# Performance work log

Hardware: AMD Instinct MI355X
Metric: run time of the kernel (lower is better)

Reference implementation:

```python
import jax, jax.numpy as jnp
import numpy as np

NEG = 1e9  # mask value added to already-selected positions (original uses -1e9)


def setup_inputs() -> dict:
    key = jax.random.key(0)
    ks = jax.random.split(key, 12)
    B, N, M = 8, 2048, 256
    s = 0.05  # keep gates/softmax in a sane range
    return dict(
        node_embedding=jax.random.normal(ks[0], (B, N, M), dtype=jnp.float32),
        z_g=jax.random.normal(ks[1], (B, M), dtype=jnp.float32) * s,
        decoder_init=jax.random.normal(ks[2], (M,), dtype=jnp.float32) * s,
        hidden0=jax.random.normal(ks[3], (M,), dtype=jnp.float32) * s,
        w_ih=jax.random.normal(ks[4], (4 * M, M), dtype=jnp.float32) * s,
        w_hh=jax.random.normal(ks[5], (4 * M, M), dtype=jnp.float32) * s,
        b_ih=jax.random.normal(ks[6], (4 * M,), dtype=jnp.float32) * s,
        b_hh=jax.random.normal(ks[7], (4 * M,), dtype=jnp.float32) * s,
        Wq=jax.random.normal(ks[8], (M, M), dtype=jnp.float32) * s,
        bq=jax.random.normal(ks[9], (M,), dtype=jnp.float32) * s,
        Wk=jax.random.normal(ks[10], (M, M), dtype=jnp.float32) * s,
        bk=jax.random.normal(ks[11], (M,), dtype=jnp.float32) * s,
    )


def reference(node_embedding, z_g, decoder_init, hidden0,
              w_ih, w_hh, b_ih, b_hh, Wq, bq, Wk, bk):
    # Returns the per-step masked softmax attention distributions [B, N, N]
    # (row t = distribution over boxes at decode step t; argmax of each row
    #  is the predicted order, and selected indices are masked out).
    N = node_embedding.shape[1]
    # LSTM input is the constant decoder_init every step -> precompute its proj.
    x_proj = decoder_init @ w_ih.T + b_ih  # [4M]

    def decode_one(z_g_b, node_emb_b):
        keys = node_emb_b @ Wk.T + bk  # [N, M] (self.key(node_embedding))

        def step(carry, _):
            h, c, used = carry
            # torch LSTMCell: gates ordered (i, f, g, o)
            gates = x_proj + h @ w_hh.T + b_hh  # [4M]
            i_g, f_g, g_g, o_g = jnp.split(gates, 4)
            i_g = jax.nn.sigmoid(i_g)
            f_g = jax.nn.sigmoid(f_g)
            g_g = jnp.tanh(g_g)
            o_g = jax.nn.sigmoid(o_g)
            c = f_g * c + i_g * g_g
            h = o_g * jnp.tanh(c)
            q = h @ Wq.T + bq                    # [M]
            scores = keys @ q                    # [N]
            scores = jnp.where(used, scores - NEG, scores)  # mask selected
            probs = jax.nn.softmax(scores)       # [N]
            idx = jnp.argmax(probs)              # top-1 pointer selection
            used = used.at[idx].set(True)
            return (h, c, used), probs

        init = (hidden0, z_g_b, jnp.zeros((N,), dtype=bool))
        _, probs = jax.lax.scan(step, init, None, length=N)
        return probs  # [N, N]

    return jax.vmap(decode_one)(z_g, node_embedding)  # [B, N, N]
```

## Files before the change

### kernel.cpp

```cpp
#include <hip/hip_runtime.h>
#include <cstdint>
#include <cstddef>

#define NB 8
#define NN 2048
#define MM 256

typedef unsigned long long u64;

__device__ __forceinline__ unsigned mapf(float f) {
  unsigned u = __float_as_uint(f + 0.f);
  return ((int)u >= 0) ? (u ^ 0x80000000u) : ~u;
}
__device__ __forceinline__ u64 shflx_u64(u64 v, int m) {
  unsigned lo = (unsigned)__shfl_xor((int)(unsigned)v, m);
  unsigned hi = (unsigned)__shfl_xor((int)(v >> 32), m);
  return ((u64)hi << 32) | lo;
}

__global__ __launch_bounds__(1024) void lstm_kernel(
    const float* __restrict__ z_g, const float* __restrict__ dec,
    const float* __restrict__ h0, const float* __restrict__ w_ih,
    const float* __restrict__ w_hh, const float* __restrict__ b_ih,
    const float* __restrict__ b_hh, const float* __restrict__ Wq,
    const float* __restrict__ bq, float* __restrict__ Qout,
    u64* __restrict__ Hslow)
{
  const int b = blockIdx.x;
  const int j = blockIdx.y;
  const int tid = threadIdx.x;
  const int w = tid >> 6;
  const int lane = tid & 63;
  const int q = w & 7;
  const int rg = w >> 3;
  const int lr = rg * 64 + lane;
  const int g = lr >> 5;
  const int mi = lr & 31;
  const int grow = g * 256 + 32 * j + mi;

  __shared__ __align__(16) float part[2][8][128];
  __shared__ __align__(16) float part2[2][32][33];

  float wreg[32];
  {
    const float* wr = w_hh + (size_t)grow * MM + 32 * q;
    #pragma unroll
    for (int i = 0; i < 8; ++i) {
      float4 v = *(const float4*)(wr + 4 * i);
      wreg[4 * i + 0] = v.x; wreg[4 * i + 1] = v.y;
      wreg[4 * i + 2] = v.z; wreg[4 * i + 3] = v.w;
    }
  }
  float wqa[8];
  {
    const float* wr = Wq + (size_t)(32 * j + mi) * MM + 32 * q + 8 * g;
    float4 w0 = *(const float4*)(wr);
    float4 w1 = *(const float4*)(wr + 4);
    wqa[0] = w0.x; wqa[1] = w0.y; wqa[2] = w0.z; wqa[3] = w0.w;
    wqa[4] = w1.x; wqa[5] = w1.y; wqa[6] = w1.z; wqa[7] = w1.w;
  }
  const float bqv = (w == 1 && lane < 32) ? bq[32 * j + lane] : 0.f;

  {
    float p = 0.f;
    const float* wr = w_ih + (size_t)grow * MM + 32 * q;
    #pragma unroll
    for (int i = 0; i < 8; ++i) {
      float4 wv = *(const float4*)(wr + 4 * i);
      float4 dv = *(const float4*)(dec + 32 * q + 4 * i);
      p += wv.x * dv.x + wv.y * dv.y + wv.z * dv.z + wv.w * dv.w;
    }
    part[0][q][lr] = p;
  }
  __syncthreads();

  float xbA = 0.f, xbB = 0.f, c_my = 0.f;
  if (w == 0) {
    #pragma unroll
    for (int rr = 0; rr < 2; ++rr) {
      const int lr2 = lane + rr * 64;
      const int g2 = lr2 >> 5, mi2 = lr2 & 31;
      const int grow2 = g2 * 256 + 32 * j + mi2;
      float xb = b_ih[grow2] + b_hh[grow2];
      #pragma unroll
      for (int qq = 0; qq < 8; ++qq) xb += part[0][qq][lr2];
      if (rr == 0) xbA = xb; else xbB = xb;
    }
    if (lane < 32) c_my = z_g[b * MM + 32 * j + lane];
  }
  __syncthreads();

  u64* Hs = Hslow + (size_t)b * 512;
  const int hidx = 32 * q + (lane & 31);

  for (int t = 0; t <= NN; ++t) {
    int hvi;
    if (t == 0) {
      hvi = __float_as_int(h0[hidx]);
    } else {
      const int off = ((t & 1) << 8) + hidx;
      u64 v = __hip_atomic_load(Hs + off, __ATOMIC_RELAXED,
                                __HIP_MEMORY_SCOPE_AGENT);
      for (;;) {
        if (__all((int)((unsigned)(v >> 32) == (unsigned)t))) break;
        v = __hip_atomic_load(Hs + off, __ATOMIC_RELAXED,
                              __HIP_MEMORY_SCOPE_AGENT);
      }
      hvi = (int)(unsigned)v;
    }

    {
      float a0 = 0.f, a1 = 0.f, a2 = 0.f, a3 = 0.f;
      #pragma unroll
      for (int k = 0; k < 32; k += 4) {
        a0 = fmaf(__uint_as_float((unsigned)__builtin_amdgcn_readlane(hvi, k + 0)), wreg[k + 0], a0);
        a1 = fmaf(__uint_as_float((unsigned)__builtin_amdgcn_readlane(hvi, k + 1)), wreg[k + 1], a1);
        a2 = fmaf(__uint_as_float((unsigned)__builtin_amdgcn_readlane(hvi, k + 2)), wreg[k + 2], a2);
        a3 = fmaf(__uint_as_float((unsigned)__builtin_amdgcn_readlane(hvi, k + 3)), wreg[k + 3], a3);
      }
      part[t & 1][q][lr] = (a0 + a1) + (a2 + a3);
    }

    {
      float qa = 0.f;
      #pragma unroll
      for (int i = 0; i < 8; ++i) {
        const float hh = __uint_as_float((unsigned)__shfl(hvi, 8 * g + i));
        qa = fmaf(hh, wqa[i], qa);
      }
      if (t > 0) part2[t & 1][g * 8 + q][mi] = qa;
    }
    __syncthreads();

    if (w == 0 && t < NN) {
      float vA = xbA, vB = xbB;
      #pragma unroll
      for (int qq = 0; qq < 8; ++qq) {
        vA += part[t & 1][qq][lane];
        vB += part[t & 1][qq][lane + 64];
      }
      const float s1 = 1.f / (1.f + __expf(-vA));
      const float e  = __expf(((lane < 32) ? -2.f : -1.f) * vB);
      const float s2 = (lane < 32) ? (2.f / (1.f + e) - 1.f)
                                   : (1.f / (1.f + e));
      const float fo1 = __shfl_xor(s1, 32);
      const float fo2 = __shfl_xor(s2, 32);
      if (lane < 32) {
        c_my = fo1 * c_my + s1 * s2;
        const float e2 = __expf(-2.f * c_my);
        const float hn = fo2 * (2.f / (1.f + e2) - 1.f);
        const u64 pk = ((u64)(unsigned)(t + 1) << 32) | (u64)__float_as_uint(hn);
        const int so = (((t + 1) & 1) << 8) + 32 * j + lane;
        __hip_atomic_store(Hs + so, pk, __ATOMIC_RELAXED,
                           __HIP_MEMORY_SCOPE_AGENT);
      }
    }

    if (w == 1 && t > 0 && lane < 32) {
      float s = 0.f;
      #pragma unroll
      for (int p = 0; p < 32; ++p) s += part2[t & 1][p][lane];
      Qout[((size_t)b * NN + (t - 1)) * MM + 32 * j + lane] = s + bqv;
    }
  }
}

__global__ __launch_bounds__(256) void gemm128(
    const float* __restrict__ A, const float* __restrict__ B,
    float* __restrict__ C, const float* __restrict__ bias,
    int K, int Ncol, long sA, long sB, long sC)
{
  __shared__ __align__(16) float As[32][132];
  __shared__ __align__(16) float Bs[32][132];
  const int tid = threadIdx.x;
  const int tx = tid & 15;
  const int ty = tid >> 4;
  const int row0 = blockIdx.y * 128;
  const int col0 = blockIdx.x * 128;
  const float* Ab = A + (size_t)blockIdx.z * (size_t)sA;
  const float* Bb = B + (size_t)blockIdx.z * (size_t)sB;
  float* Cb = C + (size_t)blockIdx.z * (size_t)sC;

  float acc[8][8];
  #pragma unroll
  for (int i = 0; i < 8; ++i)
    #pragma unroll
    for (int jj = 0; jj < 8; ++jj) acc[i][jj] = 0.f;

  for (int k0 = 0; k0 < K; k0 += 32) {
    #pragma unroll
    for (int it = 0; it < 4; ++it) {
      const int idx = tid + it * 256;
      const int r = idx >> 3;
      const int c4 = (idx & 7) << 2;
      float4 va = *(const float4*)(Ab + (size_t)(row0 + r) * K + k0 + c4);
      float4 vb = *(const float4*)(Bb + (size_t)(col0 + r) * K + k0 + c4);
      As[c4 + 0][r] = va.x; As[c4 + 1][r] = va.y;
      As[c4 + 2][r] = va.z; As[c4 + 3][r] = va.w;
      Bs[c4 + 0][r] = vb.x; Bs[c4 + 1][r] = vb.y;
      Bs[c4 + 2][r] = vb.z; Bs[c4 + 3][r] = vb.w;
    }
    __syncthreads();
    #pragma unroll
    for (int kk = 0; kk < 32; ++kk) {
      float4 a0 = *(const float4*)&As[kk][ty * 4];
      float4 a1 = *(const float4*)&As[kk][64 + ty * 4];
      float4 b0 = *(const float4*)&Bs[kk][tx * 4];
      float4 b1 = *(const float4*)&Bs[kk][64 + tx * 4];
      const float av[8] = {a0.x, a0.y, a0.z, a0.w, a1.x, a1.y, a1.z, a1.w};
      const float bv[8] = {b0.x, b0.y, b0.z, b0.w, b1.x, b1.y, b1.z, b1.w};
      #pragma unroll
      for (int i = 0; i < 8; ++i)
        #pragma unroll
        for (int jj = 0; jj < 8; ++jj)
          acc[i][jj] = fmaf(av[i], bv[jj], acc[i][jj]);
    }
    __syncthreads();
  }

  #pragma unroll
  for (int i = 0; i < 8; ++i) {
    const int r = row0 + ((i < 4) ? (ty * 4 + i) : (64 + ty * 4 + i - 4));
    float* cp = Cb + (size_t)r * Ncol + col0;
    float4 o0, o1;
    float* o0p = &o0.x; float* o1p = &o1.x;
    #pragma unroll
    for (int jj = 0; jj < 4; ++jj) {
      float v0 = acc[i][jj], v1 = acc[i][jj + 4];
      if (bias) {
        v0 += bias[col0 + tx * 4 + jj];
        v1 += bias[col0 + 64 + tx * 4 + jj];
      }
      o0p[jj] = v0; o1p[jj] = v1;
    }
    *(float4*)(cp + tx * 4) = o0;
    *(float4*)(cp + 64 + tx * 4) = o1;
  }
}

__global__ __launch_bounds__(512) void select_block(
    const float* __restrict__ S, int* __restrict__ sel)
{
  const int b = blockIdx.x;
  const int tid = threadIdx.x;
  const int w = tid >> 6;
  const int lane = tid & 63;
  const float* Sb = S + (size_t)b * NN * NN + 4 * tid;
  int* selb = sel + b * NN;

  __shared__ u64 partial[2][8];

  for (int i = tid; i < NN; i += 512) selb[i] = 0x7fffffff;
  __syncthreads();

  unsigned mybits = 0;
  const unsigned base = 2047u - 4u * (unsigned)tid;

  auto stepf = [&](float4 v, int t) {
    u64 k0 = (mybits & 1u) ? 0 : (((u64)mapf(v.x) << 32) | (base - 0u));
    u64 k1 = (mybits & 2u) ? 0 : (((u64)mapf(v.y) << 32) | (base - 1u));
    u64 k2 = (mybits & 4u) ? 0 : (((u64)mapf(v.z) << 32) | (base - 2u));
    u64 k3 = (mybits & 8u) ? 0 : (((u64)mapf(v.w) << 32) | (base - 3u));
    u64 k = k0 > k1 ? k0 : k1;
    if (k2 > k) k = k2;
    if (k3 > k) k = k3;
    #pragma unroll
    for (int off = 1; off < 64; off <<= 1) {
      u64 o = shflx_u64(k, off);
      if (o > k) k = o;
    }
    if (lane == 0) partial[t & 1][w] = k;
    __syncthreads();
    u64 pk = partial[t & 1][lane & 7];
    #pragma unroll
    for (int off = 1; off < 8; off <<= 1) {
      u64 o = shflx_u64(pk, off);
      if (o > pk) pk = o;
    }
    const int idx = 2047 - (int)(pk & 0x7ff);
    if ((idx >> 2) == tid) mybits |= 1u << (idx & 3);
    if (tid == 0) selb[idx] = t;
  };

  float4 r0 = *(const float4*)(Sb + (size_t)0 * NN);
  float4 r1 = *(const float4*)(Sb + (size_t)1 * NN);
  float4 r2 = *(const float4*)(Sb + (size_t)2 * NN);
  float4 r3 = *(const float4*)(Sb + (size_t)3 * NN);
  for (int t = 0; t < NN; t += 4) {
    const size_t p4 = (size_t)((t + 4 < NN) ? t + 4 : NN - 1) * NN;
    const size_t p5 = (size_t)((t + 5 < NN) ? t + 5 : NN - 1) * NN;
    const size_t p6 = (size_t)((t + 6 < NN) ? t + 6 : NN - 1) * NN;
    const size_t p7 = (size_t)((t + 7 < NN) ? t + 7 : NN - 1) * NN;
    stepf(r0, t);     r0 = *(const float4*)(Sb + p4);
    stepf(r1, t + 1); r1 = *(const float4*)(Sb + p5);
    stepf(r2, t + 2); r2 = *(const float4*)(Sb + p6);
    stepf(r3, t + 3); r3 = *(const float4*)(Sb + p7);
  }
}

__global__ __launch_bounds__(256) void softmax_kernel(
    float* __restrict__ out, const int* __restrict__ sel)
{
  const int t = blockIdx.x;
  const int b = blockIdx.y;
  const int tid = threadIdx.x;
  float* row = out + ((size_t)b * NN + t) * NN;
  const int* selb = sel + b * NN;
  __shared__ float red[8];

  float v[8];
  int sl[8];
  #pragma unroll
  for (int u = 0; u < 2; ++u) {
    float4 f = *(const float4*)(row + u * 1024 + tid * 4);
    int4 s4 = *(const int4*)(selb + u * 1024 + tid * 4);
    v[u * 4 + 0] = f.x; v[u * 4 + 1] = f.y; v[u * 4 + 2] = f.z; v[u * 4 + 3] = f.w;
    sl[u * 4 + 0] = s4.x; sl[u * 4 + 1] = s4.y; sl[u * 4 + 2] = s4.z; sl[u * 4 + 3] = s4.w;
  }

  float mx = -3.0e38f;
  #pragma unroll
  for (int e = 0; e < 8; ++e)
    if (sl[e] >= t) mx = fmaxf(mx, v[e]);
  #pragma unroll
  for (int off = 1; off < 64; off <<= 1) mx = fmaxf(mx, __shfl_xor(mx, off));
  if ((tid & 63) == 0) red[tid >> 6] = mx;
  __syncthreads();
  mx = fmaxf(fmaxf(red[0], red[1]), fmaxf(red[2], red[3]));

  float e8[8];
  float sum = 0.f;
  #pragma unroll
  for (int e = 0; e < 8; ++e) {
    float ex = (sl[e] >= t) ? __expf(v[e] - mx) : 0.f;
    e8[e] = ex;
    sum += ex;
  }
  #pragma unroll
  for (int off = 1; off < 64; off <<= 1) sum += __shfl_xor(sum, off);
  if ((tid & 63) == 0) red[4 + (tid >> 6)] = sum;
  __syncthreads();
  sum = red[4] + red[5] + red[6] + red[7];
  const float inv = 1.f / sum;

  #pragma unroll
  for (int u = 0; u < 2; ++u) {
    float4 o;
    o.x = e8[u * 4 + 0] * inv; o.y = e8[u * 4 + 1] * inv;
    o.z = e8[u * 4 + 2] * inv; o.w = e8[u * 4 + 3] * inv;
    *(float4*)(row + u * 1024 + tid * 4) = o;
  }
}

extern "C" void kernel_launch(void* const* d_in, const int* in_sizes, int n_in,
                              void* d_out, int out_size, void* d_ws, size_t ws_size,
                              hipStream_t stream)
{
  (void)in_sizes; (void)n_in; (void)out_size; (void)ws_size;
  const float* emb  = (const float*)d_in[0];
  const float* z_g  = (const float*)d_in[1];
  const float* dec  = (const float*)d_in[2];
  const float* h0   = (const float*)d_in[3];
  const float* w_ih = (const float*)d_in[4];
  const float* w_hh = (const float*)d_in[5];
  const float* b_ih = (const float*)d_in[6];
  const float* b_hh = (const float*)d_in[7];
  const float* Wq   = (const float*)d_in[8];
  const float* bq   = (const float*)d_in[9];
  const float* Wk   = (const float*)d_in[10];
  const float* bk   = (const float*)d_in[11];
  float* out = (float*)d_out;
  float* ws  = (float*)d_ws;

  float* keys  = ws;
  float* Q     = ws + 4194304;
  u64*   Hslow = (u64*)(ws + 8396800);
  int*   sel   = (int*)(ws + 8404992);

  lstm_kernel<<<dim3(NB, 8), 1024, 0, stream>>>(
      z_g, dec, h0, w_ih, w_hh, b_ih, b_hh, Wq, bq, Q, Hslow);

  gemm128<<<dim3(MM / 128, (NB * NN) / 128, 1), 256, 0, stream>>>(
      emb, Wk, keys, bk, MM, MM, 0, 0, 0);

  gemm128<<<dim3(NN / 128, NN / 128, NB), 256, 0, stream>>>(
      Q, keys, out, nullptr, MM, NN,
      (long)NN * MM, (long)NN * MM, (long)NN * NN);

  select_block<<<NB, 512, 0, stream>>>(out, sel);

  softmax_kernel<<<dim3(NN, NB), 256, 0, stream>>>(out, sel);
}
```

Measured before the change: 5.035 ms.

## Map LSTM blocks to XCCs so each batch syncs through the local L2

Each block reads its hardware XCC id, publishes it, and blocks are reassigned so the 8 blocks of each batch sample sit on the same XCC when possible. Those groups exchange the hidden state through a second buffer, using plain stores and sc0 loads that stay in the XCC-local L2, instead of agent-scope atomics that go through the device-coherent path. The per-step cross-block handoff latency of the 2048-step recurrence is the target. Slow-path fallbacks remain, and the new code relies on undocumented cache-coherence behaviour and on every block being resident at once for the spin barrier.

```diff
diff --git a/kernel.cpp b/kernel.cpp
--- a/kernel.cpp
+++ b/kernel.cpp
@@ -16,6 +16,16 @@
   unsigned lo = (unsigned)__shfl_xor((int)(unsigned)v, m);
   unsigned hi = (unsigned)__shfl_xor((int)(v >> 32), m);
   return ((u64)hi << 32) | lo;
+}
+
+__device__ __forceinline__ u64 load_sc0(const u64* p) {
+  u64 v;
+  asm volatile("global_load_dwordx2 %0, %1, off sc0\n\ts_waitcnt vmcnt(0)"
+               : "=v"(v) : "v"(p) : "memory");
+  return v;
+}
+__device__ __forceinline__ void store_plain(u64* p, u64 v) {
+  asm volatile("global_store_dwordx2 %0, %1, off" :: "v"(p), "v"(v) : "memory");
 }
 
 __global__ __launch_bounds__(1024) void lstm_kernel(
@@ -24,13 +34,76 @@
     const float* __restrict__ w_hh, const float* __restrict__ b_ih,
     const float* __restrict__ b_hh, const float* __restrict__ Wq,
     const float* __restrict__ bq, float* __restrict__ Qout,
-    u64* __restrict__ Hslow)
+    u64* __restrict__ Hfast, u64* __restrict__ Hslow,
+    unsigned* __restrict__ xccmap)
 {
-  const int b = blockIdx.x;
-  const int j = blockIdx.y;
+  const int flat = blockIdx.x;
   const int tid = threadIdx.x;
   const int w = tid >> 6;
   const int lane = tid & 63;
+
+  unsigned myxcc;
+  asm volatile("s_getreg_b32 %0, hwreg(HW_REG_XCC_ID)" : "=s"(myxcc));
+  myxcc &= 7u;
+  if (tid == 0)
+    __hip_atomic_store(&xccmap[flat], myxcc, __ATOMIC_RELAXED,
+                       __HIP_MEMORY_SCOPE_AGENT);
+  unsigned mv;
+  for (;;) {
+    mv = __hip_atomic_load(&xccmap[lane], __ATOMIC_RELAXED,
+                           __HIP_MEMORY_SCOPE_AGENT);
+    if (__all((int)(mv != 0xFFFFFFFFu))) break;
+  }
+  mv &= 7u;
+
+  u64 bal[8];
+  #pragma unroll
+  for (int x = 0; x < 8; ++x) bal[x] = __ballot((int)(mv == (unsigned)x));
+
+  const u64 below_me = ((u64)1 << flat) - 1;
+  int acc8 = 0, my_r = 0, my_nb = 0, my_base = 0;
+  #pragma unroll
+  for (int x = 0; x < 8; ++x) {
+    int nb = __popcll(bal[x]) >> 3;
+    const int room = 8 - acc8;
+    if (nb > room) nb = room;
+    if ((unsigned)x == myxcc) {
+      my_r = __popcll(bal[x] & below_me);
+      my_nb = nb; my_base = acc8;
+    }
+    acc8 += nb;
+  }
+
+  int b, j, fastmode;
+  if (my_r < 8 * my_nb) {
+    b = my_base + (my_r >> 3);
+    j = my_r & 7;
+    fastmode = 1;
+  } else if (acc8 < 8) {
+    const u64 below_l = ((u64)1 << lane) - 1;
+    u64 balm = bal[0];
+    #pragma unroll
+    for (int x = 1; x < 8; ++x) balm = (mv == (unsigned)x) ? bal[x] : balm;
+    const int rl = __popcll(balm & below_l);
+    int acc2 = 0, nb_l = 0;
+    #pragma unroll
+    for (int x = 0; x < 8; ++x) {
+      int nb = __popcll(bal[x]) >> 3;
+      const int room = 8 - acc2;
+      if (nb > room) nb = room;
+      if ((unsigned)x == mv) nb_l = nb;
+      acc2 += nb;
+    }
+    const u64 sm = __ballot((int)(rl >= 8 * nb_l));
+    const int sr = __popcll(sm & below_me);
+    b = acc8 + (sr >> 3);
+    j = sr & 7;
+    fastmode = 0;
+    if (b >= 8) return;
+  } else {
+    return;
+  }
+
   const int q = w & 7;
   const int rg = w >> 3;
   const int lr = rg * 64 + lane;
@@ -90,6 +163,7 @@
   }
   __syncthreads();
 
+  u64* Hf = Hfast + (size_t)b * 512;
   u64* Hs = Hslow + (size_t)b * 512;
   const int hidx = 32 * q + (lane & 31);
 
@@ -97,12 +171,23 @@
     int hvi;
     if (t == 0) {
       hvi = __float_as_int(h0[hidx]);
+    } else if (fastmode) {
+      const int off = ((t & 1) << 8) + hidx;
+      u64 v = load_sc0(Hf + off);
+      int tries = 0;
+      while (!__all((int)((unsigned)(v >> 32) == (unsigned)t))) {
+        ++tries;
+        v = ((tries & 15) == 15)
+                ? __hip_atomic_load(Hs + off, __ATOMIC_RELAXED,
+                                    __HIP_MEMORY_SCOPE_AGENT)
+                : load_sc0(Hf + off);
+      }
+      hvi = (int)(unsigned)v;
     } else {
       const int off = ((t & 1) << 8) + hidx;
       u64 v = __hip_atomic_load(Hs + off, __ATOMIC_RELAXED,
                                 __HIP_MEMORY_SCOPE_AGENT);
-      for (;;) {
-        if (__all((int)((unsigned)(v >> 32) == (unsigned)t))) break;
+      while (!__all((int)((unsigned)(v >> 32) == (unsigned)t))) {
         v = __hip_atomic_load(Hs + off, __ATOMIC_RELAXED,
                               __HIP_MEMORY_SCOPE_AGENT);
       }
@@ -151,6 +236,7 @@
         const float hn = fo2 * (2.f / (1.f + e2) - 1.f);
         const u64 pk = ((u64)(unsigned)(t + 1) << 32) | (u64)__float_as_uint(hn);
         const int so = (((t + 1) & 1) << 8) + 32 * j + lane;
+        if (fastmode) store_plain(Hf + so, pk);
         __hip_atomic_store(Hs + so, pk, __ATOMIC_RELAXED,
                            __HIP_MEMORY_SCOPE_AGENT);
       }
@@ -372,13 +458,17 @@
   float* out = (float*)d_out;
   float* ws  = (float*)d_ws;
 
-  float* keys  = ws;
-  float* Q     = ws + 4194304;
-  u64*   Hslow = (u64*)(ws + 8396800);
-  int*   sel   = (int*)(ws + 8404992);
-
-  lstm_kernel<<<dim3(NB, 8), 1024, 0, stream>>>(
-      z_g, dec, h0, w_ih, w_hh, b_ih, b_hh, Wq, bq, Q, Hslow);
+  float* keys    = ws;
+  float* Q       = ws + 4194304;
+  u64*   Hfast   = (u64*)(ws + 8388608);
+  u64*   Hslow   = (u64*)(ws + 8396800);
+  int*   sel     = (int*)(ws + 8404992);
+  unsigned* xccm = (unsigned*)(ws + 8421376);
+
+  hipMemsetAsync(xccm, 0xFF, 64 * sizeof(unsigned), stream);
+
+  lstm_kernel<<<64, 1024, 0, stream>>>(
+      z_g, dec, h0, w_ih, w_hh, b_ih, b_hh, Wq, bq, Q, Hfast, Hslow, xccm);
 
   gemm128<<<dim3(MM / 128, (NB * NN) / 128, 1), 256, 0, stream>>>(
       emb, Wk, keys, bk, MM, MM, 0, 0, 0);
```

After: 8.000 ms. 1.59x slower.

## Repartition LSTM recurrence by input slice and exchange partial gate sums across blocks

Applied to the files above, without the earlier changes.

The old version exchanged finished hidden-state slices between blocks each step. The new version has each block own a 32-wide slice of h and compute partial gate sums for all 1024 gate rows. The partial sums are exchanged through a tagged global buffer, and every block then reduces and applies the LSTM cell for its own hidden slice. Partial Q products are written to the output buffer as scratch, and a new qreduce kernel adds them up with the bias. Each step now carries more cross-block traffic (1024 values per block) but needs only one global exchange per step. The change also adds a memset and an extra kernel.

```diff
diff --git a/kernel.cpp b/kernel.cpp
--- a/kernel.cpp
+++ b/kernel.cpp
@@ -23,27 +23,20 @@
     const float* __restrict__ h0, const float* __restrict__ w_ih,
     const float* __restrict__ w_hh, const float* __restrict__ b_ih,
     const float* __restrict__ b_hh, const float* __restrict__ Wq,
-    const float* __restrict__ bq, float* __restrict__ Qout,
-    u64* __restrict__ Hslow)
+    float* __restrict__ PQ, u64* __restrict__ Pbuf)
 {
   const int b = blockIdx.x;
-  const int j = blockIdx.y;
+  const int q = blockIdx.y;
   const int tid = threadIdx.x;
-  const int w = tid >> 6;
-  const int lane = tid & 63;
-  const int q = w & 7;
-  const int rg = w >> 3;
-  const int lr = rg * 64 + lane;
-  const int g = lr >> 5;
-  const int mi = lr & 31;
-  const int grow = g * 256 + 32 * j + mi;
-
-  __shared__ __align__(16) float part[2][8][128];
-  __shared__ __align__(16) float part2[2][32][33];
+
+  __shared__ __align__(16) float hbuf[32];
+  __shared__ __align__(16) float pp[8][128];
+  __shared__ __align__(16) float act[128];
+  __shared__ __align__(16) float qq[4][256];
 
   float wreg[32];
   {
-    const float* wr = w_hh + (size_t)grow * MM + 32 * q;
+    const float* wr = w_hh + (size_t)tid * MM + 32 * q;
     #pragma unroll
     for (int i = 0; i < 8; ++i) {
       float4 v = *(const float4*)(wr + 4 * i);
@@ -51,118 +44,149 @@
       wreg[4 * i + 2] = v.z; wreg[4 * i + 3] = v.w;
     }
   }
-  float wqa[8];
+  const int m8 = tid & 255;
+  const int seg = tid >> 8;
+  float wq8[8];
   {
-    const float* wr = Wq + (size_t)(32 * j + mi) * MM + 32 * q + 8 * g;
+    const float* wr = Wq + (size_t)m8 * MM + 32 * q + 8 * seg;
     float4 w0 = *(const float4*)(wr);
     float4 w1 = *(const float4*)(wr + 4);
-    wqa[0] = w0.x; wqa[1] = w0.y; wqa[2] = w0.z; wqa[3] = w0.w;
-    wqa[4] = w1.x; wqa[5] = w1.y; wqa[6] = w1.z; wqa[7] = w1.w;
-  }
-  const float bqv = (w == 1 && lane < 32) ? bq[32 * j + lane] : 0.f;
+    wq8[0] = w0.x; wq8[1] = w0.y; wq8[2] = w0.z; wq8[3] = w0.w;
+    wq8[4] = w1.x; wq8[5] = w1.y; wq8[6] = w1.z; wq8[7] = w1.w;
+  }
+
+  const int s = tid >> 7;
+  const int idx = tid & 127;
+  const int crow = ((idx >> 5) << 8) + 32 * q + (idx & 31);
 
   {
+    const float* wr = w_ih + (size_t)crow * MM + 32 * s;
     float p = 0.f;
-    const float* wr = w_ih + (size_t)grow * MM + 32 * q;
     #pragma unroll
     for (int i = 0; i < 8; ++i) {
       float4 wv = *(const float4*)(wr + 4 * i);
-      float4 dv = *(const float4*)(dec + 32 * q + 4 * i);
+      float4 dv = *(const float4*)(dec + 32 * s + 4 * i);
       p += wv.x * dv.x + wv.y * dv.y + wv.z * dv.z + wv.w * dv.w;
     }
-    part[0][q][lr] = p;
-  }
-  __syncthreads();
-
-  float xbA = 0.f, xbB = 0.f, c_my = 0.f;
-  if (w == 0) {
-    #pragma unroll
-    for (int rr = 0; rr < 2; ++rr) {
-      const int lr2 = lane + rr * 64;
-      const int g2 = lr2 >> 5, mi2 = lr2 & 31;
-      const int grow2 = g2 * 256 + 32 * j + mi2;
-      float xb = b_ih[grow2] + b_hh[grow2];
+    pp[s][idx] = p;
+  }
+  __syncthreads();
+  float xb = 0.f, c_my = 0.f;
+  if (tid < 128) {
+    xb = b_ih[crow] + b_hh[crow];
+    #pragma unroll
+    for (int ss = 0; ss < 8; ++ss) xb += pp[ss][tid];
+  }
+  if (tid < 32) {
+    c_my = z_g[b * MM + 32 * q + tid];
+    hbuf[tid] = h0[32 * q + tid];
+  }
+  __syncthreads();
+
+  u64* Pb = Pbuf + (size_t)b * 8 * 1024;
+  const size_t parstep = (size_t)NB * 8 * 1024;
+
+  for (int t = 0; t < NN; ++t) {
+    const int par = (t + 1) & 1;
+    const float4* h4 = (const float4*)hbuf;
+
+    float a0 = 0.f, a1 = 0.f, a2 = 0.f, a3 = 0.f;
+    #pragma unroll
+    for (int i = 0; i < 8; ++i) {
+      float4 hv = h4[i];
+      a0 = fmaf(hv.x, wreg[4 * i + 0], a0);
+      a1 = fmaf(hv.y, wreg[4 * i + 1], a1);
+      a2 = fmaf(hv.z, wreg[4 * i + 2], a2);
+      a3 = fmaf(hv.w, wreg[4 * i + 3], a3);
+    }
+    const float psum = (a0 + a1) + (a2 + a3);
+
+    const u64 pk = ((u64)(unsigned)(t + 1) << 32) | (u64)__float_as_uint(psum);
+    __hip_atomic_store(Pb + par * parstep + (size_t)q * 1024 + tid, pk,
+                       __ATOMIC_RELAXED, __HIP_MEMORY_SCOPE_AGENT);
+
+    const u64* pa = Pb + par * parstep + (size_t)s * 1024 + crow;
+    u64 v = __hip_atomic_load(pa, __ATOMIC_RELAXED, __HIP_MEMORY_SCOPE_AGENT);
+
+    {
+      float4 hA = h4[2 * seg], hB = h4[2 * seg + 1];
+      float qa = wq8[0] * hA.x;
+      qa = fmaf(wq8[1], hA.y, qa); qa = fmaf(wq8[2], hA.z, qa);
+      qa = fmaf(wq8[3], hA.w, qa); qa = fmaf(wq8[4], hB.x, qa);
+      qa = fmaf(wq8[5], hB.y, qa); qa = fmaf(wq8[6], hB.z, qa);
+      qa = fmaf(wq8[7], hB.w, qa);
+      qq[seg][m8] = qa;
+    }
+
+    {
+      bool ok = ((unsigned)(v >> 32) == (unsigned)(t + 1));
+      while (!__all((int)ok)) {
+        if (!ok) {
+          v = __hip_atomic_load(pa, __ATOMIC_RELAXED,
+                                __HIP_MEMORY_SCOPE_AGENT);
+          ok = ((unsigned)(v >> 32) == (unsigned)(t + 1));
+        }
+      }
+    }
+    pp[s][idx] = __uint_as_float((unsigned)v);
+    __syncthreads();
+
+    if (tid < 128) {
+      float gsum = xb;
       #pragma unroll
-      for (int qq = 0; qq < 8; ++qq) xb += part[0][qq][lr2];
-      if (rr == 0) xbA = xb; else xbB = xb;
-    }
-    if (lane < 32) c_my = z_g[b * MM + 32 * j + lane];
-  }
-  __syncthreads();
-
-  u64* Hs = Hslow + (size_t)b * 512;
-  const int hidx = 32 * q + (lane & 31);
-
-  for (int t = 0; t <= NN; ++t) {
-    int hvi;
-    if (t == 0) {
-      hvi = __float_as_int(h0[hidx]);
-    } else {
-      const int off = ((t & 1) << 8) + hidx;
-      u64 v = __hip_atomic_load(Hs + off, __ATOMIC_RELAXED,
-                                __HIP_MEMORY_SCOPE_AGENT);
-      for (;;) {
-        if (__all((int)((unsigned)(v >> 32) == (unsigned)t))) break;
-        v = __hip_atomic_load(Hs + off, __ATOMIC_RELAXED,
-                              __HIP_MEMORY_SCOPE_AGENT);
-      }
-      hvi = (int)(unsigned)v;
-    }
-
-    {
-      float a0 = 0.f, a1 = 0.f, a2 = 0.f, a3 = 0.f;
-      #pragma unroll
-      for (int k = 0; k < 32; k += 4) {
-        a0 = fmaf(__uint_as_float((unsigned)__builtin_amdgcn_readlane(hvi, k + 0)), wreg[k + 0], a0);
-        a1 = fmaf(__uint_as_float((unsigned)__builtin_amdgcn_readlane(hvi, k + 1)), wreg[k + 1], a1);
-        a2 = fmaf(__uint_as_float((unsigned)__builtin_amdgcn_readlane(hvi, k + 2)), wreg[k + 2], a2);
-        a3 = fmaf(__uint_as_float((unsigned)__builtin_amdgcn_readlane(hvi, k + 3)), wreg[k + 3], a3);
-      }
-      part[t & 1][q][lr] = (a0 + a1) + (a2 + a3);
-    }
-
-    {
-      float qa = 0.f;
-      #pragma unroll
-      for (int i = 0; i < 8; ++i) {
-        const float hh = __uint_as_float((unsigned)__shfl(hvi, 8 * g + i));
-        qa = fmaf(hh, wqa[i], qa);
-      }
-      if (t > 0) part2[t & 1][g * 8 + q][mi] = qa;
-    }
-    __syncthreads();
-
-    if (w == 0 && t < NN) {
-      float vA = xbA, vB = xbB;
-      #pragma unroll
-      for (int qq = 0; qq < 8; ++qq) {
-        vA += part[t & 1][qq][lane];
-        vB += part[t & 1][qq][lane + 64];
-      }
-      const float s1 = 1.f / (1.f + __expf(-vA));
-      const float e  = __expf(((lane < 32) ? -2.f : -1.f) * vB);
-      const float s2 = (lane < 32) ? (2.f / (1.f + e) - 1.f)
-                                   : (1.f / (1.f + e));
-      const float fo1 = __shfl_xor(s1, 32);
-      const float fo2 = __shfl_xor(s2, 32);
-      if (lane < 32) {
-        c_my = fo1 * c_my + s1 * s2;
-        const float e2 = __expf(-2.f * c_my);
-        const float hn = fo2 * (2.f / (1.f + e2) - 1.f);
-        const u64 pk = ((u64)(unsigned)(t + 1) << 32) | (u64)__float_as_uint(hn);
-        const int so = (((t + 1) & 1) << 8) + 32 * j + lane;
-        __hip_atomic_store(Hs + so, pk, __ATOMIC_RELAXED,
-                           __HIP_MEMORY_SCOPE_AGENT);
-      }
-    }
-
-    if (w == 1 && t > 0 && lane < 32) {
-      float s = 0.f;
-      #pragma unroll
-      for (int p = 0; p < 32; ++p) s += part2[t & 1][p][lane];
-      Qout[((size_t)b * NN + (t - 1)) * MM + 32 * j + lane] = s + bqv;
-    }
-  }
+      for (int ss = 0; ss < 8; ++ss) gsum += pp[ss][tid];
+      const int g = tid >> 5;
+      float a;
+      if (g == 2) { const float e = __expf(-2.f * gsum); a = 2.f / (1.f + e) - 1.f; }
+      else        { a = 1.f / (1.f + __expf(-gsum)); }
+      act[tid] = a;
+    } else if (tid >= 256 && tid < 512 && t > 0) {
+      const int m2 = tid - 256;
+      const float qs = qq[0][m2] + qq[1][m2] + qq[2][m2] + qq[3][m2];
+      PQ[(((size_t)b * NN + (t - 1)) * 8 + q) * 256 + m2] = qs;
+    }
+    __syncthreads();
+
+    if (tid < 32) {
+      const float i_g = act[tid], f_g = act[32 + tid];
+      const float g_g = act[64 + tid], o_g = act[96 + tid];
+      c_my = f_g * c_my + i_g * g_g;
+      const float e2 = __expf(-2.f * c_my);
+      hbuf[tid] = o_g * (2.f / (1.f + e2) - 1.f);
+    }
+    __syncthreads();
+  }
+
+  {
+    const float4* h4 = (const float4*)hbuf;
+    float4 hA = h4[2 * seg], hB = h4[2 * seg + 1];
+    float qa = wq8[0] * hA.x;
+    qa = fmaf(wq8[1], hA.y, qa); qa = fmaf(wq8[2], hA.z, qa);
+    qa = fmaf(wq8[3], hA.w, qa); qa = fmaf(wq8[4], hB.x, qa);
+    qa = fmaf(wq8[5], hB.y, qa); qa = fmaf(wq8[6], hB.z, qa);
+    qa = fmaf(wq8[7], hB.w, qa);
+    qq[seg][m8] = qa;
+  }
+  __syncthreads();
+  if (tid >= 256 && tid < 512) {
+    const int m2 = tid - 256;
+    const float qs = qq[0][m2] + qq[1][m2] + qq[2][m2] + qq[3][m2];
+    PQ[(((size_t)b * NN + (NN - 1)) * 8 + q) * 256 + m2] = qs;
+  }
+}
+
+__global__ __launch_bounds__(256) void qreduce(
+    const float* __restrict__ PQ, const float* __restrict__ bq,
+    float* __restrict__ Q)
+{
+  const int t = blockIdx.x;
+  const int b = blockIdx.y;
+  const int m = threadIdx.x;
+  const float* p = PQ + (((size_t)b * NN + t) * 8) * 256 + m;
+  float s = bq[m];
+  #pragma unroll
+  for (int ss = 0; ss < 8; ++ss) s += p[ss * 256];
+  Q[((size_t)b * NN + t) * MM + m] = s;
 }
 
 __global__ __launch_bounds__(256) void gemm128(
@@ -374,11 +398,16 @@
 
   float* keys  = ws;
   float* Q     = ws + 4194304;
-  u64*   Hslow = (u64*)(ws + 8396800);
-  int*   sel   = (int*)(ws + 8404992);
+  u64*   Pbuf  = (u64*)(ws + 8388608);
+  int*   sel   = (int*)(ws + 8650752);
+  float* PQ    = out;
+
+  hipMemsetAsync(Pbuf, 0, 131072 * sizeof(u64), stream);
 
   lstm_kernel<<<dim3(NB, 8), 1024, 0, stream>>>(
-      z_g, dec, h0, w_ih, w_hh, b_ih, b_hh, Wq, bq, Q, Hslow);
+      z_g, dec, h0, w_ih, w_hh, b_ih, b_hh, Wq, PQ, Pbuf);
+
+  qreduce<<<dim3(NN, NB), 256, 0, stream>>>(PQ, bq, Q);
 
   gemm128<<<dim3(MM / 128, (NB * NN) / 128, 1), 256, 0, stream>>>(
       emb, Wk, keys, bk, MM, MM, 0, 0, 0);
```

New measurement: 5.832 ms. 1.16x slower.

## Move query projection out of LSTM recurrence into batched GEMM; restructure LSTM step

Applied to the files above, without the earlier changes.

The LSTM kernel no longer computes the Wq projection inside the serial recurrence. It writes every hidden state into a scratch area (the output buffer), and a separate gemm128 launch then computes Q = H·Wq^T + bq for all steps at once. The per-step matvec is also reorganised: each block handles one 32-column slice for all four gates, reads h from shared memory with rotated float4 indexing, and reduces with 8-lane shuffles. Four waves poll the flag buffer instead of all waves, and the flag buffer is zeroed with a memset first. This shortens the serial critical path, at the cost of an extra GEMM launch and an extra round trip of H through memory.

```diff
diff --git a/kernel.cpp b/kernel.cpp
--- a/kernel.cpp
+++ b/kernel.cpp
@@ -22,145 +22,104 @@
     const float* __restrict__ z_g, const float* __restrict__ dec,
     const float* __restrict__ h0, const float* __restrict__ w_ih,
     const float* __restrict__ w_hh, const float* __restrict__ b_ih,
-    const float* __restrict__ b_hh, const float* __restrict__ Wq,
-    const float* __restrict__ bq, float* __restrict__ Qout,
-    u64* __restrict__ Hslow)
+    const float* __restrict__ b_hh, float* __restrict__ Hall,
+    u64* __restrict__ Pbuf)
 {
   const int b = blockIdx.x;
-  const int j = blockIdx.y;
+  const int q = blockIdx.y;
   const int tid = threadIdx.x;
   const int w = tid >> 6;
   const int lane = tid & 63;
-  const int q = w & 7;
-  const int rg = w >> 3;
-  const int lr = rg * 64 + lane;
+  const int rr = lane >> 3;
+  const int c8 = lane & 7;
+  const int lr = 8 * w + rr;
   const int g = lr >> 5;
-  const int mi = lr & 31;
-  const int grow = g * 256 + 32 * j + mi;
-
-  __shared__ __align__(16) float part[2][8][128];
-  __shared__ __align__(16) float part2[2][32][33];
+  const int m = lr & 31;
+  const int grow = g * 256 + 32 * q + m;
+
+  __shared__ __align__(16) float hbuf[256];
+  __shared__ __align__(16) float act[128];
 
   float wreg[32];
   {
-    const float* wr = w_hh + (size_t)grow * MM + 32 * q;
-    #pragma unroll
-    for (int i = 0; i < 8; ++i) {
-      float4 v = *(const float4*)(wr + 4 * i);
-      wreg[4 * i + 0] = v.x; wreg[4 * i + 1] = v.y;
-      wreg[4 * i + 2] = v.z; wreg[4 * i + 3] = v.w;
-    }
-  }
-  float wqa[8];
+    const float* wr = w_hh + (size_t)grow * MM + 32 * c8;
+    #pragma unroll
+    for (int jj = 0; jj < 8; ++jj) {
+      float4 v = *(const float4*)(wr + 4 * ((jj + c8) & 7));
+      wreg[4 * jj + 0] = v.x; wreg[4 * jj + 1] = v.y;
+      wreg[4 * jj + 2] = v.z; wreg[4 * jj + 3] = v.w;
+    }
+  }
+
+  float xb;
   {
-    const float* wr = Wq + (size_t)(32 * j + mi) * MM + 32 * q + 8 * g;
-    float4 w0 = *(const float4*)(wr);
-    float4 w1 = *(const float4*)(wr + 4);
-    wqa[0] = w0.x; wqa[1] = w0.y; wqa[2] = w0.z; wqa[3] = w0.w;
-    wqa[4] = w1.x; wqa[5] = w1.y; wqa[6] = w1.z; wqa[7] = w1.w;
-  }
-  const float bqv = (w == 1 && lane < 32) ? bq[32 * j + lane] : 0.f;
-
-  {
+    const float* wr = w_ih + (size_t)grow * MM + 32 * c8;
     float p = 0.f;
-    const float* wr = w_ih + (size_t)grow * MM + 32 * q;
     #pragma unroll
     for (int i = 0; i < 8; ++i) {
       float4 wv = *(const float4*)(wr + 4 * i);
-      float4 dv = *(const float4*)(dec + 32 * q + 4 * i);
+      float4 dv = *(const float4*)(dec + 32 * c8 + 4 * i);
       p += wv.x * dv.x + wv.y * dv.y + wv.z * dv.z + wv.w * dv.w;
     }
-    part[0][q][lr] = p;
-  }
-  __syncthreads();
-
-  float xbA = 0.f, xbB = 0.f, c_my = 0.f;
-  if (w == 0) {
-    #pragma unroll
-    for (int rr = 0; rr < 2; ++rr) {
-      const int lr2 = lane + rr * 64;
-      const int g2 = lr2 >> 5, mi2 = lr2 & 31;
-      const int grow2 = g2 * 256 + 32 * j + mi2;
-      float xb = b_ih[grow2] + b_hh[grow2];
-      #pragma unroll
-      for (int qq = 0; qq < 8; ++qq) xb += part[0][qq][lr2];
-      if (rr == 0) xbA = xb; else xbB = xb;
-    }
-    if (lane < 32) c_my = z_g[b * MM + 32 * j + lane];
-  }
-  __syncthreads();
-
-  u64* Hs = Hslow + (size_t)b * 512;
-  const int hidx = 32 * q + (lane & 31);
-
-  for (int t = 0; t <= NN; ++t) {
-    int hvi;
-    if (t == 0) {
-      hvi = __float_as_int(h0[hidx]);
-    } else {
-      const int off = ((t & 1) << 8) + hidx;
-      u64 v = __hip_atomic_load(Hs + off, __ATOMIC_RELAXED,
+    p += __shfl_xor(p, 1); p += __shfl_xor(p, 2); p += __shfl_xor(p, 4);
+    xb = p + b_ih[grow] + b_hh[grow];
+  }
+
+  float c_my = 0.f;
+  if (tid < 32) c_my = z_g[b * MM + 32 * q + tid];
+  if (tid < 256) hbuf[tid] = h0[tid];
+
+  u64* Pb = Pbuf + (size_t)b * 512;
+  float* Hb = Hall + (size_t)b * NN * MM + 32 * q;
+
+  for (int tt = 0; tt < NN; ++tt) {
+    if (tt > 0 && w < 4) {
+      const int widx = (w << 6) + lane;
+      const u64* pa = Pb + ((tt & 1) << 8) + widx;
+      u64 v = __hip_atomic_load(pa, __ATOMIC_RELAXED,
                                 __HIP_MEMORY_SCOPE_AGENT);
-      for (;;) {
-        if (__all((int)((unsigned)(v >> 32) == (unsigned)t))) break;
-        v = __hip_atomic_load(Hs + off, __ATOMIC_RELAXED,
-                              __HIP_MEMORY_SCOPE_AGENT);
+      bool ok = ((unsigned)(v >> 32) == (unsigned)tt);
+      while (!__all((int)ok)) {
+        if (!ok) {
+          v = __hip_atomic_load(pa, __ATOMIC_RELAXED,
+                                __HIP_MEMORY_SCOPE_AGENT);
+          ok = ((unsigned)(v >> 32) == (unsigned)tt);
+        }
       }
-      hvi = (int)(unsigned)v;
-    }
-
-    {
-      float a0 = 0.f, a1 = 0.f, a2 = 0.f, a3 = 0.f;
-      #pragma unroll
-      for (int k = 0; k < 32; k += 4) {
-        a0 = fmaf(__uint_as_float((unsigned)__builtin_amdgcn_readlane(hvi, k + 0)), wreg[k + 0], a0);
-        a1 = fmaf(__uint_as_float((unsigned)__builtin_amdgcn_readlane(hvi, k + 1)), wreg[k + 1], a1);
-        a2 = fmaf(__uint_as_float((unsigned)__builtin_amdgcn_readlane(hvi, k + 2)), wreg[k + 2], a2);
-        a3 = fmaf(__uint_as_float((unsigned)__builtin_amdgcn_readlane(hvi, k + 3)), wreg[k + 3], a3);
-      }
-      part[t & 1][q][lr] = (a0 + a1) + (a2 + a3);
-    }
-
-    {
-      float qa = 0.f;
-      #pragma unroll
-      for (int i = 0; i < 8; ++i) {
-        const float hh = __uint_as_float((unsigned)__shfl(hvi, 8 * g + i));
-        qa = fmaf(hh, wqa[i], qa);
-      }
-      if (t > 0) part2[t & 1][g * 8 + q][mi] = qa;
-    }
-    __syncthreads();
-
-    if (w == 0 && t < NN) {
-      float vA = xbA, vB = xbB;
-      #pragma unroll
-      for (int qq = 0; qq < 8; ++qq) {
-        vA += part[t & 1][qq][lane];
-        vB += part[t & 1][qq][lane + 64];
-      }
-      const float s1 = 1.f / (1.f + __expf(-vA));
-      const float e  = __expf(((lane < 32) ? -2.f : -1.f) * vB);
-      const float s2 = (lane < 32) ? (2.f / (1.f + e) - 1.f)
-                                   : (1.f / (1.f + e));
-      const float fo1 = __shfl_xor(s1, 32);
-      const float fo2 = __shfl_xor(s2, 32);
-      if (lane < 32) {
-        c_my = fo1 * c_my + s1 * s2;
-        const float e2 = __expf(-2.f * c_my);
-        const float hn = fo2 * (2.f / (1.f + e2) - 1.f);
-        const u64 pk = ((u64)(unsigned)(t + 1) << 32) | (u64)__float_as_uint(hn);
-        const int so = (((t + 1) & 1) << 8) + 32 * j + lane;
-        __hip_atomic_store(Hs + so, pk, __ATOMIC_RELAXED,
-                           __HIP_MEMORY_SCOPE_AGENT);
-      }
-    }
-
-    if (w == 1 && t > 0 && lane < 32) {
-      float s = 0.f;
-      #pragma unroll
-      for (int p = 0; p < 32; ++p) s += part2[t & 1][p][lane];
-      Qout[((size_t)b * NN + (t - 1)) * MM + 32 * j + lane] = s + bqv;
+      hbuf[widx] = __uint_as_float((unsigned)v);
+    }
+    __syncthreads();
+
+    float a0 = 0.f, a1 = 0.f, a2 = 0.f, a3 = 0.f;
+    const float4* h4 = (const float4*)hbuf;
+    #pragma unroll
+    for (int jj = 0; jj < 8; ++jj) {
+      float4 hv = h4[8 * c8 + ((jj + c8) & 7)];
+      a0 = fmaf(hv.x, wreg[4 * jj + 0], a0);
+      a1 = fmaf(hv.y, wreg[4 * jj + 1], a1);
+      a2 = fmaf(hv.z, wreg[4 * jj + 2], a2);
+      a3 = fmaf(hv.w, wreg[4 * jj + 3], a3);
+    }
+    float s = (a0 + a1) + (a2 + a3);
+    s += __shfl_xor(s, 1); s += __shfl_xor(s, 2); s += __shfl_xor(s, 4);
+    const float gsum = s + xb;
+
+    float a;
+    if ((w >> 2) == 2) { const float e = __expf(-2.f * gsum); a = 2.f / (1.f + e) - 1.f; }
+    else               { a = 1.f / (1.f + __expf(-gsum)); }
+    if (c8 == 0) act[lr] = a;
+    __syncthreads();
+
+    if (tid < 32) {
+      const float i_g = act[tid], f_g = act[32 + tid];
+      const float g_g = act[64 + tid], o_g = act[96 + tid];
+      c_my = f_g * c_my + i_g * g_g;
+      const float e2 = __expf(-2.f * c_my);
+      const float hn = o_g * (2.f / (1.f + e2) - 1.f);
+      const u64 pk = ((u64)(unsigned)(tt + 1) << 32) | (u64)__float_as_uint(hn);
+      __hip_atomic_store(Pb + (((tt + 1) & 1) << 8) + 32 * q + tid, pk,
+                         __ATOMIC_RELAXED, __HIP_MEMORY_SCOPE_AGENT);
+      Hb[(size_t)tt * MM + tid] = hn;
     }
   }
 }
@@ -374,11 +333,17 @@
 
   float* keys  = ws;
   float* Q     = ws + 4194304;
-  u64*   Hslow = (u64*)(ws + 8396800);
-  int*   sel   = (int*)(ws + 8404992);
+  u64*   Pbuf  = (u64*)(ws + 8388608);
+  int*   sel   = (int*)(ws + 8396800);
+  float* Hall  = out;
+
+  hipMemsetAsync(Pbuf, 0, 4096 * sizeof(u64), stream);
 
   lstm_kernel<<<dim3(NB, 8), 1024, 0, stream>>>(
-      z_g, dec, h0, w_ih, w_hh, b_ih, b_hh, Wq, bq, Q, Hslow);
+      z_g, dec, h0, w_ih, w_hh, b_ih, b_hh, Hall, Pbuf);
+
+  gemm128<<<dim3(MM / 128, (NB * NN) / 128, 1), 256, 0, stream>>>(
+      Hall, Wq, Q, bq, MM, MM, 0, 0, 0);
 
   gemm128<<<dim3(MM / 128, (NB * NN) / 128, 1), 256, 0, stream>>>(
       emb, Wk, keys, bk, MM, MM, 0, 0, 0);
```

After: 4.808 ms. 1.05x faster.
